# Optimization experiments

Hardware: AMD Instinct MI355X
Metric: run time of the kernel (lower is better)

## Reference

```python
import jax, jax.numpy as jnp
import numpy as np

B, C, H, W = 16, 512, 32, 32
KC = C // 8  # key_channels = 64


def setup_inputs() -> dict:
    key = jax.random.key(0)
    ks = jax.random.split(key, 6)
    s_in = 1.0 / np.sqrt(C)
    return {
        "x": jax.random.normal(ks[0], (B, C, H, W), dtype=jnp.float32),
        "Wq": jax.random.normal(ks[1], (KC, C), dtype=jnp.float32) * s_in,
        "bq": jnp.zeros((KC,), dtype=jnp.float32),
        "Wk": jax.random.normal(ks[2], (KC, C), dtype=jnp.float32) * s_in,
        "bk": jnp.zeros((KC,), dtype=jnp.float32),
        "Wv": jax.random.normal(ks[3], (C, C), dtype=jnp.float32) * s_in,
        "bv": jnp.zeros((C,), dtype=jnp.float32),
        "Wo": jax.random.normal(ks[4], (C, C), dtype=jnp.float32) * s_in,
        "bo": jnp.zeros((C,), dtype=jnp.float32),
        "gamma": jnp.zeros((1,), dtype=jnp.float32),
    }


def reference(x, Wq, bq, Wk, bk, Wv, bv, Wo, bo, gamma):
    b, c, h, w = x.shape
    n = h * w
    kc = Wq.shape[0]
    xf = x.reshape(b, c, n)  # [B, C, N]
    # 1x1 convs == channel matmuls
    q = jnp.einsum('kc,bcn->bnk', Wq, xf) + bq  # [B, N, KC]
    k = jnp.einsum('kc,bcn->bkn', Wk, xf) + bk[None, :, None]  # [B, KC, N]
    v = jnp.einsum('vc,bcn->bnv', Wv, xf) + bv  # [B, N, C]
    scale = jnp.asarray(kc, x.dtype) ** -0.5
    att = jax.nn.softmax(jnp.einsum('bnk,bkm->bnm', q, k) * scale, axis=-1)  # [B, N, N]
    out = jnp.einsum('bnm,bmv->bnv', att, v)  # [B, N, C]
    out = jnp.einsum('cv,bnv->bcn', Wo, out) + bo[None, :, None]  # [B, C, N]
    out = gamma[0] * out + xf
    return out.reshape(b, c, h, w)
```

## Files before the change

kernel.cpp:

```cpp
#include <hip/hip_runtime.h>
#include <cstddef>


typedef unsigned short ushort_t;
typedef __attribute__((ext_vector_type(8))) short bf16x8;
typedef __attribute__((ext_vector_type(4))) float f32x4;

__device__ __forceinline__ ushort_t f2bf(float f) {
  unsigned int x = __float_as_uint(f);
  unsigned int r = (x + 0x7fffu + ((x >> 16) & 1u)) >> 16;
  return (ushort_t)r;
}

template <int TM>
__device__ __forceinline__ void gemm_core(
    const ushort_t* __restrict__ A, int lda,
    const ushort_t* __restrict__ B, int ldb,
    int K, int m0, int n0,
    ushort_t* As, ushort_t* Bs, f32x4 (*acc)[4])
{
  constexpr int MT  = TM / 32;
  constexpr int WTM = TM / 2;
  const int t = threadIdx.x;
  const int lane = t & 63, quad = lane >> 4, l15 = lane & 15;
  const int w = t >> 6, wm = w >> 1, wn = w & 1;

  #pragma unroll
  for (int i = 0; i < MT; ++i)
    #pragma unroll
    for (int j = 0; j < 4; ++j) acc[i][j] = (f32x4){0.f, 0.f, 0.f, 0.f};

  for (int k0 = 0; k0 < K; k0 += 64) {
    #pragma unroll
    for (int i = 0; i < TM / 32; ++i) {
      const int s = i * 256 + t, m = s >> 3, g = s & 7;
      const uint4 v = *(const uint4*)(A + (size_t)(m0 + m) * lda + k0 + g * 8);
      *(uint4*)(As + m * 72 + g * 8) = v;
    }
    #pragma unroll
    for (int i = 0; i < 4; ++i) {
      const int s = i * 256 + t, m = s >> 3, g = s & 7;
      const uint4 v = *(const uint4*)(B + (size_t)(n0 + m) * ldb + k0 + g * 8);
      *(uint4*)(Bs + m * 72 + g * 8) = v;
    }
    __syncthreads();
    #pragma unroll
    for (int kk = 0; kk < 2; ++kk) {
      const int gq = kk * 4 + quad;
      bf16x8 af[MT], bfr[4];
      #pragma unroll
      for (int i = 0; i < MT; ++i)
        af[i] = *(const bf16x8*)(As + (wm * WTM + i * 16 + l15) * 72 + gq * 8);
      #pragma unroll
      for (int j = 0; j < 4; ++j)
        bfr[j] = *(const bf16x8*)(Bs + (wn * 64 + j * 16 + l15) * 72 + gq * 8);
      #pragma unroll
      for (int i = 0; i < MT; ++i)
        #pragma unroll
        for (int j = 0; j < 4; ++j)
          acc[i][j] = __builtin_amdgcn_mfma_f32_16x16x32_bf16(
              af[i], bfr[j], acc[i][j], 0, 0, 0);
    }
    __syncthreads();
  }
}

template <int TM, class F>
__device__ __forceinline__ void store_bf16(
    ushort_t* lds, ushort_t* __restrict__ out, int ldo, int m0, int n0,
    f32x4 (*acc)[4], F f)
{
  constexpr int MT = TM / 32, WTM = TM / 2, SI = TM / 16;
  const int t = threadIdx.x;
  const int lane = t & 63, quad = lane >> 4, l15 = lane & 15;
  const int w = t >> 6, wm = w >> 1, wn = w & 1;
  #pragma unroll
  for (int i = 0; i < MT; ++i)
    #pragma unroll
    for (int j = 0; j < 4; ++j)
      #pragma unroll
      for (int r = 0; r < 4; ++r) {
        const int rl = wm * WTM + i * 16 + quad * 4 + r;
        const int cl = wn * 64 + j * 16 + l15;
        lds[rl * 136 + cl] = f2bf(f(i, j, r, rl, cl, acc[i][j][r]));
      }
  __syncthreads();
  #pragma unroll
  for (int i = 0; i < SI; ++i) {
    const int s = i * 256 + t, m = s >> 4, g = s & 15;
    const uint4 v = *(const uint4*)(lds + m * 136 + g * 8);
    *(uint4*)(out + (size_t)(m0 + m) * ldo + n0 + g * 8) = v;
  }
}

__global__ __launch_bounds__(256) void prep_x(
    const float* __restrict__ x, ushort_t* __restrict__ xbfT)
{
  __shared__ float T[64][65];
  const int t = threadIdx.x;
  const int b = blockIdx.z, c0 = blockIdx.y * 64, n0 = blockIdx.x * 64;
  const float* xb = x + ((size_t)b * 512 + c0) * 1024 + n0;
  const int nj = t & 63, ci0 = t >> 6;
  #pragma unroll
  for (int p = 0; p < 16; ++p) {
    const int ci = p * 4 + ci0;
    T[ci][nj] = xb[(size_t)ci * 1024 + nj];
  }
  __syncthreads();
  const int cl = t & 63, nr0 = t >> 6;
  #pragma unroll
  for (int p = 0; p < 16; ++p) {
    const int nr = p * 4 + nr0;
    xbfT[((size_t)b * 1024 + n0 + nr) * 512 + c0 + cl] = f2bf(T[cl][nr]);
  }
}

__global__ __launch_bounds__(256) void wcvt(
    const float* __restrict__ Wq, const float* __restrict__ Wk,
    const float* __restrict__ Wv, const float* __restrict__ Wo,
    ushort_t* __restrict__ Wqk, ushort_t* __restrict__ Wvb,
    ushort_t* __restrict__ Wob)
{
  const int i = blockIdx.x * 256 + threadIdx.x;
  if (i < 65536) {
    const float v = (i < 32768) ? Wq[i] : Wk[i - 32768];
    Wqk[i] = f2bf(v);
  } else if (i < 327680) {
    Wvb[i - 65536] = f2bf(Wv[i - 65536]);
  } else if (i < 589824) {
    Wob[i - 327680] = f2bf(Wo[i - 327680]);
  }
}

__global__ __launch_bounds__(256) void k1a_qk(
    const ushort_t* __restrict__ xbfT, const ushort_t* __restrict__ Wqk,
    const float* __restrict__ bq, const float* __restrict__ bk,
    ushort_t* __restrict__ qkt)
{
  __shared__ __align__(16) ushort_t lds[(64 + 128) * 72];
  const int b = blockIdx.z, m0 = blockIdx.y * 64;
  f32x4 acc[2][4];
  gemm_core<64>(xbfT + (size_t)b * 524288, 512, Wqk, 512, 512, m0, 0,
                lds, lds + 64 * 72, acc);
  const int t = threadIdx.x, lane = t & 63, l15 = lane & 15;
  const int w = t >> 6, wn = w & 1;
  float bc[4];
  #pragma unroll
  for (int j = 0; j < 4; ++j) {
    const int col = wn * 64 + j * 16 + l15;
    bc[j] = (col < 64) ? bq[col] : bk[col - 64];
  }
  store_bf16<64>(lds, qkt + (size_t)b * 131072, 128, m0, 0, acc,
      [&](int, int j, int, int, int, float v) { return v + bc[j]; });
}

__global__ __launch_bounds__(256) void k1b_v(
    const ushort_t* __restrict__ Wvb, const ushort_t* __restrict__ xbfT,
    const float* __restrict__ bv, ushort_t* __restrict__ vt2)
{
  __shared__ __align__(16) ushort_t lds[(128 + 128) * 72];
  const int b = blockIdx.z, m0 = blockIdx.y * 128, n0 = blockIdx.x * 128;
  f32x4 acc[4][4];
  gemm_core<128>(Wvb, 512, xbfT + (size_t)b * 524288, 512, 512, m0, n0,
                 lds, lds + 128 * 72, acc);
  const int t = threadIdx.x, lane = t & 63, quad = lane >> 4;
  const int w = t >> 6, wm = w >> 1;
  float br[4][4];
  #pragma unroll
  for (int i = 0; i < 4; ++i)
    #pragma unroll
    for (int r = 0; r < 4; ++r)
      br[i][r] = bv[m0 + wm * 64 + i * 16 + quad * 4 + r];
  store_bf16<128>(lds, vt2 + (size_t)b * 524288, 1024, m0, n0, acc,
      [&](int i, int, int r, int, int, float v) { return v + br[i][r]; });
}

__global__ __launch_bounds__(256) void k2_scores(
    const ushort_t* __restrict__ qkt, ushort_t* __restrict__ p,
    float* __restrict__ lpart)
{
  __shared__ __align__(16) ushort_t lds[(128 + 128) * 72];
  __shared__ float lsum[128][2];
  const int b = blockIdx.z, m0 = blockIdx.y * 128, c0 = blockIdx.x * 128;
  f32x4 acc[4][4];
  const ushort_t* A = qkt + (size_t)b * 131072;
  gemm_core<128>(A, 128, A + 64, 128, 64, m0, c0, lds, lds + 128 * 72, acc);
  const int t = threadIdx.x, lane = t & 63, quad = lane >> 4, l15 = lane & 15;
  const int w = t >> 6, wm = w >> 1, wn = w & 1;
  #pragma unroll
  for (int i = 0; i < 4; ++i)
    #pragma unroll
    for (int r = 0; r < 4; ++r) {
      float s = 0.f;
      #pragma unroll
      for (int j = 0; j < 4; ++j) {
        const float e = __expf(acc[i][j][r] * 0.125f);
        acc[i][j][r] = e;
        s += e;
      }
      #pragma unroll
      for (int d = 1; d < 16; d <<= 1) s += __shfl_xor(s, d);
      if (l15 == 0) lsum[wm * 64 + i * 16 + quad * 4 + r][wn] = s;
    }
  store_bf16<128>(lds, p + (size_t)b * 1048576, 1024, m0, c0, acc,
      [](int, int, int, int, int, float v) { return v; });
  if (t < 128)
    lpart[(size_t)b * 8192 + (size_t)blockIdx.x * 1024 + m0 + t] =
        lsum[t][0] + lsum[t][1];
}

__global__ void k2b_rowsum(const float* __restrict__ lpart,
                           float* __restrict__ linv)
{
  const int b = blockIdx.x, n = threadIdx.x;
  float s = 0.f;
  #pragma unroll
  for (int ct = 0; ct < 8; ++ct) s += lpart[(size_t)b * 8192 + ct * 1024 + n];
  linv[b * 1024 + n] = 1.0f / s;
}

__global__ __launch_bounds__(256) void k3_pv(
    const ushort_t* __restrict__ p, const ushort_t* __restrict__ vt2,
    const float* __restrict__ linv, ushort_t* __restrict__ o1)
{
  __shared__ __align__(16) ushort_t lds[(128 + 128) * 72];
  const int b = blockIdx.z, m0 = blockIdx.y * 128, c0 = blockIdx.x * 128;
  f32x4 acc[4][4];
  gemm_core<128>(p + (size_t)b * 1048576, 1024, vt2 + (size_t)b * 524288, 1024,
                 1024, m0, c0, lds, lds + 128 * 72, acc);
  const int t = threadIdx.x, lane = t & 63, quad = lane >> 4;
  const int w = t >> 6, wm = w >> 1;
  float li[4][4];
  #pragma unroll
  for (int i = 0; i < 4; ++i)
    #pragma unroll
    for (int r = 0; r < 4; ++r)
      li[i][r] = linv[b * 1024 + m0 + wm * 64 + i * 16 + quad * 4 + r];
  store_bf16<128>(lds, o1 + (size_t)b * 524288, 512, m0, c0, acc,
      [&](int i, int, int r, int, int, float v) { return v * li[i][r]; });
}

__global__ __launch_bounds__(256) void k4_proj(
    const ushort_t* __restrict__ Wob, const ushort_t* __restrict__ o1,
    const float* __restrict__ bo, const float* __restrict__ gamma,
    const float* __restrict__ x, float* __restrict__ out)
{
  __shared__ __align__(16) ushort_t lds[(128 + 128) * 72];
  const int b = blockIdx.z, m0 = blockIdx.y * 128, n0 = blockIdx.x * 128;
  f32x4 acc[4][4];
  gemm_core<128>(Wob, 512, o1 + (size_t)b * 524288, 512, 512, m0, n0,
                 lds, lds + 128 * 72, acc);
  const int t = threadIdx.x, lane = t & 63, quad = lane >> 4, l15 = lane & 15;
  const int w = t >> 6, wm = w >> 1, wn = w & 1;
  const float g = gamma[0];
  float br[4][4];
  #pragma unroll
  for (int i = 0; i < 4; ++i)
    #pragma unroll
    for (int r = 0; r < 4; ++r)
      br[i][r] = bo[m0 + wm * 64 + i * 16 + quad * 4 + r];
  float* fl = (float*)lds;
  #pragma unroll
  for (int h = 0; h < 2; ++h) {
    if (wm == h) {
      #pragma unroll
      for (int i = 0; i < 4; ++i)
        #pragma unroll
        for (int j = 0; j < 4; ++j)
          #pragma unroll
          for (int r = 0; r < 4; ++r)
            fl[(i * 16 + quad * 4 + r) * 132 + wn * 64 + j * 16 + l15] =
                g * (acc[i][j][r] + br[i][r]);
    }
    __syncthreads();
    #pragma unroll
    for (int i2 = 0; i2 < 8; ++i2) {
      const int s = i2 * 256 + t, m = s >> 5, c4 = s & 31;
      f32x4 v = *(const f32x4*)(fl + m * 132 + c4 * 4);
      const size_t gi = ((size_t)b * 512 + m0 + h * 64 + m) * 1024 + n0 + c4 * 4;
      const f32x4 xr = *(const f32x4*)(x + gi);
      v += xr;
      *(f32x4*)(out + gi) = v;
    }
    __syncthreads();
  }
}

extern "C" void kernel_launch(void* const* d_in, const int* in_sizes, int n_in,
                              void* d_out, int out_size, void* d_ws, size_t ws_size,
                              hipStream_t stream) {
  const float* x     = (const float*)d_in[0];
  const float* Wq    = (const float*)d_in[1];
  const float* bq    = (const float*)d_in[2];
  const float* Wk    = (const float*)d_in[3];
  const float* bk    = (const float*)d_in[4];
  const float* Wv    = (const float*)d_in[5];
  const float* bv    = (const float*)d_in[6];
  const float* Wo    = (const float*)d_in[7];
  const float* bo    = (const float*)d_in[8];
  const float* gamma = (const float*)d_in[9];
  float* out = (float*)d_out;

  char* wsp = (char*)d_ws;
  ushort_t* xbfT   = (ushort_t*)wsp;                        wsp += (size_t)16 * 1024 * 512 * 2;
  ushort_t* Wqk_bf = (ushort_t*)wsp;                        wsp += (size_t)128 * 512 * 2;
  ushort_t* Wv_bf  = (ushort_t*)wsp;                        wsp += (size_t)512 * 512 * 2;
  ushort_t* Wo_bf  = (ushort_t*)wsp;                        wsp += (size_t)512 * 512 * 2;
  ushort_t* qkt    = (ushort_t*)wsp;                        wsp += (size_t)16 * 1024 * 128 * 2;
  ushort_t* vt2    = (ushort_t*)wsp;                        wsp += (size_t)16 * 512 * 1024 * 2;
  ushort_t* p      = (ushort_t*)wsp;                        wsp += (size_t)16 * 1024 * 1024 * 2;
  float*    lpart  = (float*)wsp;                           wsp += (size_t)16 * 8 * 1024 * 4;
  float*    linv   = (float*)wsp;                           wsp += (size_t)16 * 1024 * 4;
  ushort_t* o1     = xbfT;

  prep_x   <<<dim3(16, 8, 16), 256, 0, stream>>>(x, xbfT);
  wcvt     <<<2304, 256, 0, stream>>>(Wq, Wk, Wv, Wo, Wqk_bf, Wv_bf, Wo_bf);
  k1a_qk   <<<dim3(1, 16, 16), 256, 0, stream>>>(xbfT, Wqk_bf, bq, bk, qkt);
  k1b_v    <<<dim3(8, 4, 16), 256, 0, stream>>>(Wv_bf, xbfT, bv, vt2);
  k2_scores<<<dim3(8, 8, 16), 256, 0, stream>>>(qkt, p, lpart);
  k2b_rowsum<<<16, 1024, 0, stream>>>(lpart, linv);
  k3_pv    <<<dim3(4, 8, 16), 256, 0, stream>>>(p, vt2, linv, o1);
  k4_proj  <<<dim3(8, 4, 16), 256, 0, stream>>>(Wo_bf, o1, bo, gamma, x, out);
}
```

Baseline: 197.3 us.

## Use direct global-to-LDS loads with XOR-swizzled tiles in GEMM core

The GEMM core now stages A and B tiles with global_load_lds (direct global-to-LDS DMA) instead of register round-trips. The padded 72-element row stride becomes an unpadded 64 stride with an XOR swizzle on 16-byte groups, so fragment reads stay free of bank conflicts. The LDS arrays are resized so the epilogue scratch still fits. The prep_x transpose also writes two packed bf16 values per store. The aim is to cut VGPR traffic and instruction count in the load stage, at the cost of relying on the swizzle and wave-uniform LDS base addressing being exactly correct.

```diff
diff --git a/kernel.cpp b/kernel.cpp
--- a/kernel.cpp
+++ b/kernel.cpp
@@ -10,6 +10,12 @@
   unsigned int x = __float_as_uint(f);
   unsigned int r = (x + 0x7fffu + ((x >> 16) & 1u)) >> 16;
   return (ushort_t)r;
+}
+
+__device__ __forceinline__ void gload16(const ushort_t* g, ushort_t* l) {
+  __builtin_amdgcn_global_load_lds(
+      (const __attribute__((address_space(1))) void*)g,
+      (__attribute__((address_space(3))) void*)l, 16, 0, 0);
 }
 
 template <int TM>
@@ -24,6 +30,8 @@
   const int t = threadIdx.x;
   const int lane = t & 63, quad = lane >> 4, l15 = lane & 15;
   const int w = t >> 6, wm = w >> 1, wn = w & 1;
+  const int rr = (lane >> 3) & 7;
+  const int gg = (lane & 7) ^ rr;
 
   #pragma unroll
   for (int i = 0; i < MT; ++i)
@@ -33,27 +41,28 @@
   for (int k0 = 0; k0 < K; k0 += 64) {
     #pragma unroll
     for (int i = 0; i < TM / 32; ++i) {
-      const int s = i * 256 + t, m = s >> 3, g = s & 7;
-      const uint4 v = *(const uint4*)(A + (size_t)(m0 + m) * lda + k0 + g * 8);
-      *(uint4*)(As + m * 72 + g * 8) = v;
+      const int mrow = w * (TM / 4) + i * 8;
+      gload16(A + (size_t)(m0 + mrow + rr) * lda + k0 + gg * 8,
+              As + mrow * 64);
     }
     #pragma unroll
     for (int i = 0; i < 4; ++i) {
-      const int s = i * 256 + t, m = s >> 3, g = s & 7;
-      const uint4 v = *(const uint4*)(B + (size_t)(n0 + m) * ldb + k0 + g * 8);
-      *(uint4*)(Bs + m * 72 + g * 8) = v;
+      const int mrow = w * 32 + i * 8;
+      gload16(B + (size_t)(n0 + mrow + rr) * ldb + k0 + gg * 8,
+              Bs + mrow * 64);
     }
     __syncthreads();
     #pragma unroll
     for (int kk = 0; kk < 2; ++kk) {
       const int gq = kk * 4 + quad;
+      const int sg = (gq ^ (l15 & 7)) * 8;
       bf16x8 af[MT], bfr[4];
       #pragma unroll
       for (int i = 0; i < MT; ++i)
-        af[i] = *(const bf16x8*)(As + (wm * WTM + i * 16 + l15) * 72 + gq * 8);
+        af[i] = *(const bf16x8*)(As + (wm * WTM + i * 16 + l15) * 64 + sg);
       #pragma unroll
       for (int j = 0; j < 4; ++j)
-        bfr[j] = *(const bf16x8*)(Bs + (wn * 64 + j * 16 + l15) * 72 + gq * 8);
+        bfr[j] = *(const bf16x8*)(Bs + (wn * 64 + j * 16 + l15) * 64 + sg);
       #pragma unroll
       for (int i = 0; i < MT; ++i)
         #pragma unroll
@@ -107,11 +116,13 @@
     T[ci][nj] = xb[(size_t)ci * 1024 + nj];
   }
   __syncthreads();
-  const int cl = t & 63, nr0 = t >> 6;
-  #pragma unroll
-  for (int p = 0; p < 16; ++p) {
-    const int nr = p * 4 + nr0;
-    xbfT[((size_t)b * 1024 + n0 + nr) * 512 + c0 + cl] = f2bf(T[cl][nr]);
+  const int c2 = (t & 31) * 2, nr0 = t >> 5;
+  #pragma unroll
+  for (int p = 0; p < 8; ++p) {
+    const int nr = p * 8 + nr0;
+    const unsigned lo = f2bf(T[c2][nr]), hi = f2bf(T[c2 + 1][nr]);
+    *(unsigned*)&xbfT[((size_t)b * 1024 + n0 + nr) * 512 + c0 + c2] =
+        lo | (hi << 16);
   }
 }
 
@@ -137,11 +148,11 @@
     const float* __restrict__ bq, const float* __restrict__ bk,
     ushort_t* __restrict__ qkt)
 {
-  __shared__ __align__(16) ushort_t lds[(64 + 128) * 72];
+  __shared__ __align__(16) ushort_t lds[(64 + 128) * 64];
   const int b = blockIdx.z, m0 = blockIdx.y * 64;
   f32x4 acc[2][4];
   gemm_core<64>(xbfT + (size_t)b * 524288, 512, Wqk, 512, 512, m0, 0,
-                lds, lds + 64 * 72, acc);
+                lds, lds + 64 * 64, acc);
   const int t = threadIdx.x, lane = t & 63, l15 = lane & 15;
   const int w = t >> 6, wn = w & 1;
   float bc[4];
@@ -158,11 +169,11 @@
     const ushort_t* __restrict__ Wvb, const ushort_t* __restrict__ xbfT,
     const float* __restrict__ bv, ushort_t* __restrict__ vt2)
 {
-  __shared__ __align__(16) ushort_t lds[(128 + 128) * 72];
+  __shared__ __align__(16) ushort_t lds[128 * 136];
   const int b = blockIdx.z, m0 = blockIdx.y * 128, n0 = blockIdx.x * 128;
   f32x4 acc[4][4];
   gemm_core<128>(Wvb, 512, xbfT + (size_t)b * 524288, 512, 512, m0, n0,
-                 lds, lds + 128 * 72, acc);
+                 lds, lds + 128 * 64, acc);
   const int t = threadIdx.x, lane = t & 63, quad = lane >> 4;
   const int w = t >> 6, wm = w >> 1;
   float br[4][4];
@@ -179,12 +190,12 @@
     const ushort_t* __restrict__ qkt, ushort_t* __restrict__ p,
     float* __restrict__ lpart)
 {
-  __shared__ __align__(16) ushort_t lds[(128 + 128) * 72];
+  __shared__ __align__(16) ushort_t lds[128 * 136];
   __shared__ float lsum[128][2];
   const int b = blockIdx.z, m0 = blockIdx.y * 128, c0 = blockIdx.x * 128;
   f32x4 acc[4][4];
   const ushort_t* A = qkt + (size_t)b * 131072;
-  gemm_core<128>(A, 128, A + 64, 128, 64, m0, c0, lds, lds + 128 * 72, acc);
+  gemm_core<128>(A, 128, A + 64, 128, 64, m0, c0, lds, lds + 128 * 64, acc);
   const int t = threadIdx.x, lane = t & 63, quad = lane >> 4, l15 = lane & 15;
   const int w = t >> 6, wm = w >> 1, wn = w & 1;
   #pragma unroll
@@ -223,11 +234,11 @@
     const ushort_t* __restrict__ p, const ushort_t* __restrict__ vt2,
     const float* __restrict__ linv, ushort_t* __restrict__ o1)
 {
-  __shared__ __align__(16) ushort_t lds[(128 + 128) * 72];
+  __shared__ __align__(16) ushort_t lds[128 * 136];
   const int b = blockIdx.z, m0 = blockIdx.y * 128, c0 = blockIdx.x * 128;
   f32x4 acc[4][4];
   gemm_core<128>(p + (size_t)b * 1048576, 1024, vt2 + (size_t)b * 524288, 1024,
-                 1024, m0, c0, lds, lds + 128 * 72, acc);
+                 1024, m0, c0, lds, lds + 128 * 64, acc);
   const int t = threadIdx.x, lane = t & 63, quad = lane >> 4;
   const int w = t >> 6, wm = w >> 1;
   float li[4][4];
@@ -245,11 +256,11 @@
     const float* __restrict__ bo, const float* __restrict__ gamma,
     const float* __restrict__ x, float* __restrict__ out)
 {
-  __shared__ __align__(16) ushort_t lds[(128 + 128) * 72];
+  __shared__ __align__(16) ushort_t lds[128 * 136];
   const int b = blockIdx.z, m0 = blockIdx.y * 128, n0 = blockIdx.x * 128;
   f32x4 acc[4][4];
   gemm_core<128>(Wob, 512, o1 + (size_t)b * 524288, 512, 512, m0, n0,
-                 lds, lds + 128 * 72, acc);
+                 lds, lds + 128 * 64, acc);
   const int t = threadIdx.x, lane = t & 63, quad = lane >> 4, l15 = lane & 15;
   const int w = t >> 6, wm = w >> 1, wn = w & 1;
   const float g = gamma[0];
@@ -302,23 +313,23 @@
   float* out = (float*)d_out;
 
   char* wsp = (char*)d_ws;
-  ushort_t* xbfT   = (ushort_t*)wsp;                        wsp += (size_t)16 * 1024 * 512 * 2;
-  ushort_t* Wqk_bf = (ushort_t*)wsp;                        wsp += (size_t)128 * 512 * 2;
-  ushort_t* Wv_bf  = (ushort_t*)wsp;                        wsp += (size_t)512 * 512 * 2;
-  ushort_t* Wo_bf  = (ushort_t*)wsp;                        wsp += (size_t)512 * 512 * 2;
-  ushort_t* qkt    = (ushort_t*)wsp;                        wsp += (size_t)16 * 1024 * 128 * 2;
-  ushort_t* vt2    = (ushort_t*)wsp;                        wsp += (size_t)16 * 512 * 1024 * 2;
-  ushort_t* p      = (ushort_t*)wsp;                        wsp += (size_t)16 * 1024 * 1024 * 2;
-  float*    lpart  = (float*)wsp;                           wsp += (size_t)16 * 8 * 1024 * 4;
-  float*    linv   = (float*)wsp;                           wsp += (size_t)16 * 1024 * 4;
+  ushort_t* xbfT   = (ushort_t*)wsp;  wsp += (size_t)16 * 1024 * 512 * 2;
+  ushort_t* Wqk_bf = (ushort_t*)wsp;  wsp += (size_t)128 * 512 * 2;
+  ushort_t* Wv_bf  = (ushort_t*)wsp;  wsp += (size_t)512 * 512 * 2;
+  ushort_t* Wo_bf  = (ushort_t*)wsp;  wsp += (size_t)512 * 512 * 2;
+  ushort_t* qkt    = (ushort_t*)wsp;  wsp += (size_t)16 * 1024 * 128 * 2;
+  ushort_t* vt2    = (ushort_t*)wsp;  wsp += (size_t)16 * 512 * 1024 * 2;
+  ushort_t* p      = (ushort_t*)wsp;  wsp += (size_t)16 * 1024 * 1024 * 2;
+  float*    lpart  = (float*)wsp;     wsp += (size_t)16 * 8 * 1024 * 4;
+  float*    linv   = (float*)wsp;     wsp += (size_t)16 * 1024 * 4;
   ushort_t* o1     = xbfT;
 
-  prep_x   <<<dim3(16, 8, 16), 256, 0, stream>>>(x, xbfT);
-  wcvt     <<<2304, 256, 0, stream>>>(Wq, Wk, Wv, Wo, Wqk_bf, Wv_bf, Wo_bf);
-  k1a_qk   <<<dim3(1, 16, 16), 256, 0, stream>>>(xbfT, Wqk_bf, bq, bk, qkt);
-  k1b_v    <<<dim3(8, 4, 16), 256, 0, stream>>>(Wv_bf, xbfT, bv, vt2);
-  k2_scores<<<dim3(8, 8, 16), 256, 0, stream>>>(qkt, p, lpart);
+  prep_x    <<<dim3(16, 8, 16), 256, 0, stream>>>(x, xbfT);
+  wcvt      <<<2304, 256, 0, stream>>>(Wq, Wk, Wv, Wo, Wqk_bf, Wv_bf, Wo_bf);
+  k1a_qk    <<<dim3(1, 16, 16), 256, 0, stream>>>(xbfT, Wqk_bf, bq, bk, qkt);
+  k1b_v     <<<dim3(8, 4, 16), 256, 0, stream>>>(Wv_bf, xbfT, bv, vt2);
+  k2_scores <<<dim3(8, 8, 16), 256, 0, stream>>>(qkt, p, lpart);
   k2b_rowsum<<<16, 1024, 0, stream>>>(lpart, linv);
-  k3_pv    <<<dim3(4, 8, 16), 256, 0, stream>>>(p, vt2, linv, o1);
-  k4_proj  <<<dim3(8, 4, 16), 256, 0, stream>>>(Wo_bf, o1, bo, gamma, x, out);
-}
+  k3_pv     <<<dim3(4, 8, 16), 256, 0, stream>>>(p, vt2, linv, o1);
+  k4_proj   <<<dim3(8, 4, 16), 256, 0, stream>>>(Wo_bf, o1, bo, gamma, x, out);
+}
```

After: 197.4 us. About the same (+0.1%).
